# Kernel optimization log

Measured on AMD Instinct MI355X. Metric: run time of the kernel, lower is better.

## Reference

```python
import jax, jax.numpy as jnp
import numpy as np

H = 50  # hidden_dim
L = 4   # num_layers

def setup_inputs() -> dict:
    key = jax.random.key(0)
    ks = jax.random.split(key, 12)
    B, T, D = 2048, 512, 1
    s0 = 1.0 / np.sqrt(H)  # PyTorch GRU init scale
    x = jax.random.normal(ks[0], (B, T, D), dtype=jnp.float32)
    # layer 0 (input size 1)
    W_ih0 = jax.random.uniform(ks[1], (3 * H, D), minval=-s0, maxval=s0, dtype=jnp.float32)
    W_hh0 = jax.random.uniform(ks[2], (3 * H, H), minval=-s0, maxval=s0, dtype=jnp.float32)
    b_ih0 = jax.random.uniform(ks[3], (3 * H,), minval=-s0, maxval=s0, dtype=jnp.float32)
    b_hh0 = jax.random.uniform(ks[4], (3 * H,), minval=-s0, maxval=s0, dtype=jnp.float32)
    # layers 1..3 stacked (input size H)
    W_ih = jax.random.uniform(ks[5], (L - 1, 3 * H, H), minval=-s0, maxval=s0, dtype=jnp.float32)
    W_hh = jax.random.uniform(ks[6], (L - 1, 3 * H, H), minval=-s0, maxval=s0, dtype=jnp.float32)
    b_ih = jax.random.uniform(ks[7], (L - 1, 3 * H), minval=-s0, maxval=s0, dtype=jnp.float32)
    b_hh = jax.random.uniform(ks[8], (L - 1, 3 * H), minval=-s0, maxval=s0, dtype=jnp.float32)
    fc_w = jax.random.uniform(ks[9], (1, H), minval=-s0, maxval=s0, dtype=jnp.float32)
    fc_b = jax.random.uniform(ks[10], (1,), minval=-s0, maxval=s0, dtype=jnp.float32)
    return {"x": x, "W_ih0": W_ih0, "W_hh0": W_hh0, "b_ih0": b_ih0, "b_hh0": b_hh0,
            "W_ih": W_ih, "W_hh": W_hh, "b_ih": b_ih, "b_hh": b_hh,
            "fc_w": fc_w, "fc_b": fc_b}


def _gru_layer(x_seq, Wih, Whh, bih, bhh):
    # x_seq: [B, T, Din] -> outputs [B, T, H]. PyTorch GRU cell math.
    gx = jnp.einsum('btd,gd->btg', x_seq, Wih) + bih  # [B, T, 3H], precomputed input gates
    gx = jnp.transpose(gx, (1, 0, 2))  # [T, B, 3H]
    h0 = jnp.zeros((x_seq.shape[0], H), dtype=x_seq.dtype)

    def step(h, gxt):
        gh = h @ Whh.T + bhh  # [B, 3H]
        xr, xz, xn = jnp.split(gxt, 3, axis=-1)
        hr, hz, hn = jnp.split(gh, 3, axis=-1)
        r = jax.nn.sigmoid(xr + hr)
        z = jax.nn.sigmoid(xz + hz)
        n = jnp.tanh(xn + r * hn)
        h_new = (1.0 - z) * n + z * h
        return h_new, h_new

    _, hs = jax.lax.scan(step, h0, gx)  # hs: [T, B, H]
    return jnp.transpose(hs, (1, 0, 2))  # [B, T, H]


def reference(x, W_ih0, W_hh0, b_ih0, b_hh0, W_ih, W_hh, b_ih, b_hh, fc_w, fc_b):
    out = _gru_layer(x, W_ih0, W_hh0, b_ih0, b_hh0)
    for l in range(L - 1):  # eval mode: dropout inactive
        out = _gru_layer(out, W_ih[l], W_hh[l], b_ih[l], b_hh[l])
    last = out[:, -1, :]  # [B, H]
    logits = last @ fc_w.T + fc_b  # [B, 1]
    return jax.nn.sigmoid(logits)
```

## Files before the change

### kernel.cpp

```cpp
#include <hip/hip_runtime.h>
#include <hip/hip_fp16.h>

#define HDIM  50
#define G3    150
#define TSEQ  512
#define BATCH 2048
#define NB    8
#define NLAY  4
#define NT    12

typedef _Float16 f16x8 __attribute__((ext_vector_type(8)));
typedef _Float16 f16x2 __attribute__((ext_vector_type(2)));
typedef float    f32x4 __attribute__((ext_vector_type(4)));

#define MFMA(a,b,c) __builtin_amdgcn_mfma_f32_16x16x32_f16((a),(b),(c),0,0,0)

__global__ __launch_bounds__(256, 1)
void gru_fused1w(const float* __restrict__ xin,
                 const float* __restrict__ Wih0, const float* __restrict__ Whh0,
                 const float* __restrict__ bih0, const float* __restrict__ bhh0,
                 const float* __restrict__ WihL, const float* __restrict__ WhhL,
                 const float* __restrict__ bihL, const float* __restrict__ bhhL,
                 const float* __restrict__ fcw,  const float* __restrict__ fcb,
                 float* __restrict__ out)
{
    const int tid  = threadIdx.x;
    const int lay  = tid >> 6;
    const int lane = tid & 63;
    const int lb   = lane & 15;
    const int lg   = lane >> 4;
    const int b0   = blockIdx.x * NB;
    const int lbc  = (lb < NB) ? lb : (NB - 1);

    __shared__ __align__(16) _Float16 h_lds[NLAY][2][16][72];
    __shared__ float x_row[NB][516];

    const float* Wih = (lay==0) ? Wih0 : WihL + (size_t)(lay-1)*G3*HDIM;
    const float* Whh = (lay==0) ? Whh0 : WhhL + (size_t)(lay-1)*G3*HDIM;
    const float* bih = (lay==0) ? bih0 : bihL + (lay-1)*G3;
    const float* bhh = (lay==0) ? bhh0 : bhhL + (lay-1)*G3;

    f16x8 a_hh[NT][2], a_ih[NT][2];
#pragma unroll
    for (int mt = 0; mt < NT; ++mt) {
        const int  ur = (mt & 3)*16 + lb;
        const bool rv = ur < HDIM;
        const int  gr = 50*(mt >> 2) + (rv ? ur : 0);
#pragma unroll
        for (int kt = 0; kt < 2; ++kt) {
            f16x8 fh, fi;
#pragma unroll
            for (int j = 0; j < 8; ++j) {
                const int k = 32*kt + 8*lg + j;
                float vh = 0.f, vi = 0.f;
                if (rv) {
                    if (k < HDIM)       vh = Whh[gr*HDIM + k];
                    else if (k == HDIM) vh = bhh[gr];
                    if (lay == 0) {
                        if (kt == 0 && k == 0)      vi = Wih[gr];
                        else if (kt == 0 && k == 1) vi = bih[gr];
                    } else {
                        if (k < HDIM)       vi = Wih[gr*HDIM + k];
                        else if (k == HDIM) vi = bih[gr];
                    }
                }
                fh[j] = (_Float16)vh; fi[j] = (_Float16)vi;
            }
            a_hh[mt][kt] = fh; a_ih[mt][kt] = fi;
        }
    }

    for (int k = tid; k < NB*TSEQ; k += 256)
        x_row[k >> 9][k & 511] = xin[(size_t)(b0 + (k >> 9))*TSEQ + (k & 511)];
    for (int k = tid; k < NLAY*2*16*72; k += 256)
        ((_Float16*)h_lds)[k] = (_Float16)(((k % 72) == HDIM) ? 1.f : 0.f);

    float hold[4][4];
#pragma unroll
    for (int m = 0; m < 4; ++m)
#pragma unroll
        for (int i = 0; i < 4; ++i) hold[m][i] = 0.f;
    __syncthreads();

    f16x8 bh0 = *(const f16x8*)&h_lds[lay][1][lb][8*lg];
    f16x8 bh1 = *(const f16x8*)&h_lds[lay][1][lb][32 + 8*lg];
    f16x8 bx0{}, bx1{};
    if (lay == 0) {
        const float xv = x_row[lbc][0];
#pragma unroll
        for (int j = 0; j < 8; ++j) bx0[j] = (_Float16)0.f;
        if (lg == 0) { bx0[0] = (_Float16)xv; bx0[1] = (_Float16)1.f; }
    } else {
        bx0 = *(const f16x8*)&h_lds[lay-1][1][lb][8*lg];
        bx1 = *(const f16x8*)&h_lds[lay-1][1][lb][32 + 8*lg];
    }

    for (int s = 0; s < TSEQ + NLAY - 1; ++s) {
        const int t = s - lay;
        if (t >= 0 && t < TSEQ) {
            f32x4 acc[NT], accx[4];
#pragma unroll
            for (int mt = 0; mt < NT; ++mt) acc[mt] = f32x4{0.f,0.f,0.f,0.f};
#pragma unroll
            for (int m = 0; m < 4; ++m) accx[m] = f32x4{0.f,0.f,0.f,0.f};

#pragma unroll
            for (int mt = 0; mt < NT; ++mt) acc[mt]  = MFMA(a_hh[mt][0], bh0, acc[mt]);
#pragma unroll
            for (int mt = 0; mt < 8; ++mt)  acc[mt]  = MFMA(a_ih[mt][0], bx0, acc[mt]);
#pragma unroll
            for (int m = 0; m < 4; ++m)     accx[m]  = MFMA(a_ih[8+m][0], bx0, accx[m]);
#pragma unroll
            for (int mt = 0; mt < NT; ++mt) acc[mt]  = MFMA(a_hh[mt][1], bh1, acc[mt]);
            if (lay != 0) {
#pragma unroll
                for (int mt = 0; mt < 8; ++mt) acc[mt] = MFMA(a_ih[mt][1], bx1, acc[mt]);
#pragma unroll
                for (int m = 0; m < 4; ++m)    accx[m] = MFMA(a_ih[8+m][1], bx1, accx[m]);
            }

#pragma unroll
            for (int mt = 0; mt < 8; ++mt) {
#pragma unroll
                for (int i = 0; i < 4; ++i) {
                    if (((mt & 3) == 3) && i >= 2) continue;
                    acc[mt][i] = __builtin_amdgcn_rcpf(1.f + __expf(-acc[mt][i]));
                }
            }

            _Float16* hrow = &h_lds[lay][s & 1][lb][0];
#pragma unroll
            for (int m = 0; m < 4; ++m) {
                float hp[4];
#pragma unroll
                for (int i = 0; i < 4; ++i) {
                    if (m == 3 && i >= 2) { hp[i] = 0.f; continue; }
                    const float r  = acc[m][i];
                    const float z  = acc[4+m][i];
                    const float vp = accx[m][i] + r * acc[8+m][i];
                    const float e2 = __expf(2.f * vp);
                    const float n  = 1.f - 2.f*__builtin_amdgcn_rcpf(e2 + 1.f);
                    const float h  = fmaf(z, hold[m][i] - n, n);
                    hold[m][i] = h;
                    hp[i] = h;
                }
#pragma unroll
                for (int ip = 0; ip < 2; ++ip) {
                    if (m == 3 && ip == 1) continue;
                    if (m != 3 || lg == 0) {
                        f16x2 q; q[0] = (_Float16)hp[2*ip]; q[1] = (_Float16)hp[2*ip+1];
                        *(f16x2*)&hrow[16*m + 4*lg + 2*ip] = q;
                    }
                }
            }
        }
        __syncthreads();

        const int pb = s & 1;
        bh0 = *(const f16x8*)&h_lds[lay][pb][lb][8*lg];
        bh1 = *(const f16x8*)&h_lds[lay][pb][lb][32 + 8*lg];
        if (lay == 0) {
            const int tt = (s+1 < TSEQ) ? s+1 : TSEQ-1;
            const float xv = x_row[lbc][tt];
#pragma unroll
            for (int j = 0; j < 8; ++j) bx0[j] = (_Float16)0.f;
            if (lg == 0) { bx0[0] = (_Float16)xv; bx0[1] = (_Float16)1.f; }
        } else {
            bx0 = *(const f16x8*)&h_lds[lay-1][pb][lb][8*lg];
            bx1 = *(const f16x8*)&h_lds[lay-1][pb][lb][32 + 8*lg];
        }
    }

    if (tid < NB) {
        float sacc = fcb[0];
#pragma unroll
        for (int j = 0; j < HDIM; ++j)
            sacc = fmaf((float)h_lds[NLAY-1][0][tid][j], fcw[j], sacc);
        out[b0 + tid] = __builtin_amdgcn_rcpf(1.f + __expf(-sacc));
    }
}

extern "C" void kernel_launch(void* const* d_in, const int* in_sizes, int n_in,
                              void* d_out, int out_size, void* d_ws, size_t ws_size,
                              hipStream_t stream) {
    const float* x     = (const float*)d_in[0];
    const float* W_ih0 = (const float*)d_in[1];
    const float* W_hh0 = (const float*)d_in[2];
    const float* b_ih0 = (const float*)d_in[3];
    const float* b_hh0 = (const float*)d_in[4];
    const float* W_ih  = (const float*)d_in[5];
    const float* W_hh  = (const float*)d_in[6];
    const float* b_ih  = (const float*)d_in[7];
    const float* b_hh  = (const float*)d_in[8];
    const float* fc_w  = (const float*)d_in[9];
    const float* fc_b  = (const float*)d_in[10];
    float* out = (float*)d_out;

    dim3 grid(BATCH / NB), block(256);
    gru_fused1w<<<grid, block, 0, stream>>>(
        x, W_ih0, W_hh0, b_ih0, b_hh0,
        W_ih, W_hh, b_ih, b_hh, fc_w, fc_b, out);
}
```

Measured before the change: 621.1 us.

## Replace per-step block barriers with LDS ring buffers and per-layer producer/consumer flags

Each wave, one per GRU layer, no longer waits on a block-wide __syncthreads every timestep. Hidden states now go into a 4-deep LDS ring per layer, and adjacent layers coordinate through workgroup-scope atomic prod/cons counters, so faster layers can run ahead of slower ones. The recurrent h-part MFMAs are also issued before waiting on the lower layer's output, to hide that wait, and the half-precision packing uses cvt_pkrtz, which rounds toward zero instead of to nearest. The risks are spin-wait overhead, correctness that depends on wave-level memory ordering in LDS, and reading its own previous h from the ring without an explicit barrier.

```diff
diff --git a/kernel.cpp b/kernel.cpp
--- a/kernel.cpp
+++ b/kernel.cpp
@@ -8,21 +8,25 @@
 #define NB    8
 #define NLAY  4
 #define NT    12
+#define RING  4
 
 typedef _Float16 f16x8 __attribute__((ext_vector_type(8)));
-typedef _Float16 f16x2 __attribute__((ext_vector_type(2)));
 typedef float    f32x4 __attribute__((ext_vector_type(4)));
 
 #define MFMA(a,b,c) __builtin_amdgcn_mfma_f32_16x16x32_f16((a),(b),(c),0,0,0)
 
+static __device__ inline unsigned pk2(float a, float b) {
+    return __builtin_bit_cast(unsigned, __builtin_amdgcn_cvt_pkrtz(a, b));
+}
+
 __global__ __launch_bounds__(256, 1)
-void gru_fused1w(const float* __restrict__ xin,
-                 const float* __restrict__ Wih0, const float* __restrict__ Whh0,
-                 const float* __restrict__ bih0, const float* __restrict__ bhh0,
-                 const float* __restrict__ WihL, const float* __restrict__ WhhL,
-                 const float* __restrict__ bihL, const float* __restrict__ bhhL,
-                 const float* __restrict__ fcw,  const float* __restrict__ fcb,
-                 float* __restrict__ out)
+void gru_async(const float* __restrict__ xin,
+               const float* __restrict__ Wih0, const float* __restrict__ Whh0,
+               const float* __restrict__ bih0, const float* __restrict__ bhh0,
+               const float* __restrict__ WihL, const float* __restrict__ WhhL,
+               const float* __restrict__ bihL, const float* __restrict__ bhhL,
+               const float* __restrict__ fcw,  const float* __restrict__ fcb,
+               float* __restrict__ out)
 {
     const int tid  = threadIdx.x;
     const int lay  = tid >> 6;
@@ -32,8 +36,10 @@
     const int b0   = blockIdx.x * NB;
     const int lbc  = (lb < NB) ? lb : (NB - 1);
 
-    __shared__ __align__(16) _Float16 h_lds[NLAY][2][16][72];
+    __shared__ __align__(16) _Float16 hsl[NLAY][RING][16][72];
     __shared__ float x_row[NB][516];
+    __shared__ int prod[NLAY];
+    __shared__ int cons[NLAY];
 
     const float* Wih = (lay==0) ? Wih0 : WihL + (size_t)(lay-1)*G3*HDIM;
     const float* Whh = (lay==0) ? Whh0 : WhhL + (size_t)(lay-1)*G3*HDIM;
@@ -72,110 +78,117 @@
 
     for (int k = tid; k < NB*TSEQ; k += 256)
         x_row[k >> 9][k & 511] = xin[(size_t)(b0 + (k >> 9))*TSEQ + (k & 511)];
-    for (int k = tid; k < NLAY*2*16*72; k += 256)
-        ((_Float16*)h_lds)[k] = (_Float16)(((k % 72) == HDIM) ? 1.f : 0.f);
+    for (int k = tid; k < NLAY*RING*16*72; k += 256)
+        ((_Float16*)hsl)[k] = (_Float16)(((k % 72) == HDIM) ? 1.f : 0.f);
+    if (tid < NLAY) { prod[tid] = 0; cons[tid] = 0; }
 
     float hold[4][4];
 #pragma unroll
     for (int m = 0; m < 4; ++m)
 #pragma unroll
         for (int i = 0; i < 4; ++i) hold[m][i] = 0.f;
-    __syncthreads();
-
-    f16x8 bh0 = *(const f16x8*)&h_lds[lay][1][lb][8*lg];
-    f16x8 bh1 = *(const f16x8*)&h_lds[lay][1][lb][32 + 8*lg];
+
     f16x8 bx0{}, bx1{};
     if (lay == 0) {
-        const float xv = x_row[lbc][0];
 #pragma unroll
         for (int j = 0; j < 8; ++j) bx0[j] = (_Float16)0.f;
-        if (lg == 0) { bx0[0] = (_Float16)xv; bx0[1] = (_Float16)1.f; }
-    } else {
-        bx0 = *(const f16x8*)&h_lds[lay-1][1][lb][8*lg];
-        bx1 = *(const f16x8*)&h_lds[lay-1][1][lb][32 + 8*lg];
-    }
-
-    for (int s = 0; s < TSEQ + NLAY - 1; ++s) {
-        const int t = s - lay;
-        if (t >= 0 && t < TSEQ) {
-            f32x4 acc[NT], accx[4];
-#pragma unroll
-            for (int mt = 0; mt < NT; ++mt) acc[mt] = f32x4{0.f,0.f,0.f,0.f};
-#pragma unroll
-            for (int m = 0; m < 4; ++m) accx[m] = f32x4{0.f,0.f,0.f,0.f};
-
-#pragma unroll
-            for (int mt = 0; mt < NT; ++mt) acc[mt]  = MFMA(a_hh[mt][0], bh0, acc[mt]);
-#pragma unroll
-            for (int mt = 0; mt < 8; ++mt)  acc[mt]  = MFMA(a_ih[mt][0], bx0, acc[mt]);
-#pragma unroll
-            for (int m = 0; m < 4; ++m)     accx[m]  = MFMA(a_ih[8+m][0], bx0, accx[m]);
-#pragma unroll
-            for (int mt = 0; mt < NT; ++mt) acc[mt]  = MFMA(a_hh[mt][1], bh1, acc[mt]);
-            if (lay != 0) {
-#pragma unroll
-                for (int mt = 0; mt < 8; ++mt) acc[mt] = MFMA(a_ih[mt][1], bx1, acc[mt]);
-#pragma unroll
-                for (int m = 0; m < 4; ++m)    accx[m] = MFMA(a_ih[8+m][1], bx1, accx[m]);
-            }
-
-#pragma unroll
-            for (int mt = 0; mt < 8; ++mt) {
-#pragma unroll
-                for (int i = 0; i < 4; ++i) {
-                    if (((mt & 3) == 3) && i >= 2) continue;
-                    acc[mt][i] = __builtin_amdgcn_rcpf(1.f + __expf(-acc[mt][i]));
-                }
-            }
-
-            _Float16* hrow = &h_lds[lay][s & 1][lb][0];
-#pragma unroll
-            for (int m = 0; m < 4; ++m) {
-                float hp[4];
-#pragma unroll
-                for (int i = 0; i < 4; ++i) {
-                    if (m == 3 && i >= 2) { hp[i] = 0.f; continue; }
-                    const float r  = acc[m][i];
-                    const float z  = acc[4+m][i];
-                    const float vp = accx[m][i] + r * acc[8+m][i];
-                    const float e2 = __expf(2.f * vp);
-                    const float n  = 1.f - 2.f*__builtin_amdgcn_rcpf(e2 + 1.f);
-                    const float h  = fmaf(z, hold[m][i] - n, n);
-                    hold[m][i] = h;
-                    hp[i] = h;
-                }
-#pragma unroll
-                for (int ip = 0; ip < 2; ++ip) {
-                    if (m == 3 && ip == 1) continue;
-                    if (m != 3 || lg == 0) {
-                        f16x2 q; q[0] = (_Float16)hp[2*ip]; q[1] = (_Float16)hp[2*ip+1];
-                        *(f16x2*)&hrow[16*m + 4*lg + 2*ip] = q;
-                    }
-                }
-            }
-        }
-        __syncthreads();
-
-        const int pb = s & 1;
-        bh0 = *(const f16x8*)&h_lds[lay][pb][lb][8*lg];
-        bh1 = *(const f16x8*)&h_lds[lay][pb][lb][32 + 8*lg];
+        if (lg == 0) bx0[1] = (_Float16)1.f;
+    }
+    const f32x4 Z4 = {0.f, 0.f, 0.f, 0.f};
+    __syncthreads();
+
+    for (int t = 0; t < TSEQ; ++t) {
+        const int rs = (t - 1) & (RING - 1);
+        f16x8 bh0 = *(const f16x8*)&hsl[lay][rs][lb][8*lg];
+        f16x8 bh1 = *(const f16x8*)&hsl[lay][rs][lb][32 + 8*lg];
+
+        f32x4 acc[NT], accx[4];
+#pragma unroll
+        for (int mt = 0; mt < NT; ++mt) acc[mt] = MFMA(a_hh[mt][0], bh0, Z4);
+#pragma unroll
+        for (int mt = 0; mt < NT; ++mt) acc[mt] = MFMA(a_hh[mt][1], bh1, acc[mt]);
+
         if (lay == 0) {
-            const int tt = (s+1 < TSEQ) ? s+1 : TSEQ-1;
-            const float xv = x_row[lbc][tt];
-#pragma unroll
-            for (int j = 0; j < 8; ++j) bx0[j] = (_Float16)0.f;
-            if (lg == 0) { bx0[0] = (_Float16)xv; bx0[1] = (_Float16)1.f; }
+            if (lg == 0) bx0[0] = (_Float16)x_row[lbc][t];
         } else {
-            bx0 = *(const f16x8*)&h_lds[lay-1][pb][lb][8*lg];
-            bx1 = *(const f16x8*)&h_lds[lay-1][pb][lb][32 + 8*lg];
-        }
-    }
+            const int want = t + 1;
+            while (__hip_atomic_load(&prod[lay-1], __ATOMIC_ACQUIRE,
+                                     __HIP_MEMORY_SCOPE_WORKGROUP) < want) {}
+            const int xs = t & (RING - 1);
+            bx0 = *(const f16x8*)&hsl[lay-1][xs][lb][8*lg];
+            bx1 = *(const f16x8*)&hsl[lay-1][xs][lb][32 + 8*lg];
+            if (lane == 0)
+                __hip_atomic_store(&cons[lay-1], want, __ATOMIC_RELEASE,
+                                   __HIP_MEMORY_SCOPE_WORKGROUP);
+        }
+
+#pragma unroll
+        for (int mt = 0; mt < 8; ++mt) acc[mt] = MFMA(a_ih[mt][0], bx0, acc[mt]);
+#pragma unroll
+        for (int m = 0; m < 4; ++m)    accx[m] = MFMA(a_ih[8+m][0], bx0, Z4);
+        if (lay != 0) {
+#pragma unroll
+            for (int mt = 0; mt < 8; ++mt) acc[mt] = MFMA(a_ih[mt][1], bx1, acc[mt]);
+#pragma unroll
+            for (int m = 0; m < 4; ++m)    accx[m] = MFMA(a_ih[8+m][1], bx1, accx[m]);
+        }
+
+#pragma unroll
+        for (int mt = 0; mt < 8; ++mt) {
+#pragma unroll
+            for (int i = 0; i < 4; ++i) {
+                if (((mt & 3) == 3) && i >= 2) continue;
+                acc[mt][i] = __builtin_amdgcn_rcpf(1.f + __expf(-acc[mt][i]));
+            }
+        }
+
+        float hp[4][4];
+#pragma unroll
+        for (int m = 0; m < 4; ++m) {
+#pragma unroll
+            for (int i = 0; i < 4; ++i) {
+                if (m == 3 && i >= 2) { hp[m][i] = 0.f; continue; }
+                const float r  = acc[m][i];
+                const float z  = acc[4+m][i];
+                const float vp = accx[m][i] + r * acc[8+m][i];
+                const float e2 = __expf(2.f * vp);
+                const float n  = 1.f - 2.f*__builtin_amdgcn_rcpf(e2 + 1.f);
+                const float h  = fmaf(z, hold[m][i] - n, n);
+                hold[m][i] = h;
+                hp[m][i] = h;
+            }
+        }
+
+        if (lay < NLAY-1 && t >= RING) {
+            const int need = t - RING + 1;
+            while (__hip_atomic_load(&cons[lay], __ATOMIC_ACQUIRE,
+                                     __HIP_MEMORY_SCOPE_WORKGROUP) < need) {}
+        }
+
+        {
+            _Float16* hrow = &hsl[lay][t & (RING-1)][lb][0];
+#pragma unroll
+            for (int m = 0; m < 3; ++m) {
+                uint2 q; q.x = pk2(hp[m][0], hp[m][1]);
+                         q.y = pk2(hp[m][2], hp[m][3]);
+                *(uint2*)&hrow[16*m + 4*lg] = q;
+            }
+            if (lg == 0) {
+                *(unsigned*)&hrow[48] = pk2(hp[3][0], hp[3][1]);
+            }
+        }
+        if (lane == 0)
+            __hip_atomic_store(&prod[lay], t + 1, __ATOMIC_RELEASE,
+                               __HIP_MEMORY_SCOPE_WORKGROUP);
+    }
+
+    __syncthreads();
 
     if (tid < NB) {
         float sacc = fcb[0];
 #pragma unroll
         for (int j = 0; j < HDIM; ++j)
-            sacc = fmaf((float)h_lds[NLAY-1][0][tid][j], fcw[j], sacc);
+            sacc = fmaf((float)hsl[NLAY-1][(TSEQ-1) & (RING-1)][tid][j], fcw[j], sacc);
         out[b0 + tid] = __builtin_amdgcn_rcpf(1.f + __expf(-sacc));
     }
 }
@@ -197,7 +210,7 @@
     float* out = (float*)d_out;
 
     dim3 grid(BATCH / NB), block(256);
-    gru_fused1w<<<grid, block, 0, stream>>>(
+    gru_async<<<grid, block, 0, stream>>>(
         x, W_ih0, W_hh0, b_ih0, b_hh0,
         W_ih, W_hh, b_ih, b_hh, fc_w, fc_b, out);
 }
```

Measured after the change: 689.2 us. 1.11x slower.
